# Kernel optimization log

Hardware: AMD Instinct MI355X
Metric: run time of the kernel (lower is better)

## Reference

```python
import jax, jax.numpy as jnp
import numpy as np

SHAPES = ((496, 432), (248, 216), (124, 108))
NS = (40000, 20000, 8000)
T = 32
B = 4
EPS = 1e-3


def _bn(x, g, b, m, v):
    return (x - m) * (g / jnp.sqrt(v + EPS)) + b


def _vfe_scale(voxels, num_pts, w1, p1, w2, p2):
    # voxels: (N, T, 4); num_pts: (N,)
    Tp = voxels.shape[1]
    n = num_pts.astype(voxels.dtype)[:, None, None]
    m3 = voxels[:, :, :3].sum(axis=1, keepdims=True) / n
    m2 = voxels[:, :, :2].sum(axis=1, keepdims=True) / n
    feat = jnp.concatenate([voxels[:, :, :4], voxels[:, :, :3] - m3, voxels[:, :, :2] - m2], axis=-1)  # (N,T,9)
    mask = (jnp.arange(Tp)[None, :] < num_pts[:, None]).astype(voxels.dtype)[:, :, None]
    x = feat
    for w, (g, b_, rm, rv) in ((w1, p1), (w2, p2)):
        h = jax.nn.relu(_bn(jnp.einsum('ntc,cd->ntd', x, w), g, b_, rm, rv))  # (N,T,64)
        gmax = h.max(axis=1, keepdims=True)  # global max includes padded rows, as in torch source
        x = jnp.concatenate([h, jnp.broadcast_to(gmax, h.shape)], axis=-1) * mask  # (N,T,128)
    return x.max(axis=1)[:, :64]  # (N,64)


def _scatter_bev(vf, coords, h, w, batch_size):
    b = coords[:, 0]
    y = jnp.clip(coords[:, 2], 0, h - 1)
    x = jnp.clip(coords[:, 3], 0, w - 1)
    grid = jnp.zeros((batch_size, vf.shape[1], h, w), vf.dtype)
    return grid.at[b, :, y, x].set(vf)


def _fusion(x, w, g, b, m, v):
    y = jax.lax.conv_general_dilated(x, w, (1, 1), ((1, 1), (1, 1)),
                                     dimension_numbers=('NCHW', 'OIHW', 'NCHW'))
    y = _bn(y, g[None, :, None, None], b[None, :, None, None], m[None, :, None, None], v[None, :, None, None])
    return jax.nn.relu(y)


def setup_inputs() -> dict:
    key = jax.random.key(0)
    ks = jax.random.split(key, 32)
    inp = {}
    for s in range(3):
        h, w = SHAPES[s]
        inp[f'voxels_{s}'] = jax.random.normal(ks[s], (NS[s], T, 4), dtype=jnp.float32)
        inp[f'num_pts_{s}'] = jax.random.randint(ks[3 + s], (NS[s],), 1, T + 1, dtype=jnp.int32)
        b = jax.random.randint(ks[6 + s], (NS[s],), 0, B, dtype=jnp.int32)
        z = jnp.zeros((NS[s],), jnp.int32)
        y = jax.random.randint(ks[9 + s], (NS[s],), 0, h, dtype=jnp.int32)
        x = jax.random.randint(ks[12 + s], (NS[s],), 0, w, dtype=jnp.int32)
        inp[f'coords_{s}'] = jnp.stack([b, z, y, x], axis=1)
    # VFE params (stacked across the 3 scales; identical shapes per scale)
    inp['w1'] = jax.random.normal(ks[15], (3, 9, 64), dtype=jnp.float32) * 0.1
    inp['g1'] = jnp.ones((3, 64), jnp.float32) + 0.1 * jax.random.normal(ks[16], (3, 64))
    inp['b1'] = 0.05 * jax.random.normal(ks[17], (3, 64))
    inp['rm1'] = 0.05 * jax.random.normal(ks[18], (3, 64))
    inp['rv1'] = 0.5 + jnp.abs(jax.random.normal(ks[19], (3, 64)))
    inp['w2'] = jax.random.normal(ks[20], (3, 128, 64), dtype=jnp.float32) * 0.05
    inp['g2'] = jnp.ones((3, 64), jnp.float32) + 0.1 * jax.random.normal(ks[21], (3, 64))
    inp['b2'] = 0.05 * jax.random.normal(ks[22], (3, 64))
    inp['rm2'] = 0.05 * jax.random.normal(ks[23], (3, 64))
    inp['rv2'] = 0.5 + jnp.abs(jax.random.normal(ks[24], (3, 64)))
    # Fusion convs (2): Conv2d(128,64,3) + BN
    inp['fw'] = jax.random.normal(ks[25], (2, 64, 128, 3, 3), dtype=jnp.float32) * 0.03
    inp['fg'] = jnp.ones((2, 64), jnp.float32) + 0.1 * jax.random.normal(ks[26], (2, 64))
    inp['fb'] = 0.05 * jax.random.normal(ks[27], (2, 64))
    inp['fm'] = 0.05 * jax.random.normal(ks[28], (2, 64))
    inp['fv'] = 0.5 + jnp.abs(jax.random.normal(ks[29], (2, 64)))
    inp['batch_size'] = B
    return inp


def reference(voxels_0, voxels_1, voxels_2,
              w1, g1, b1, rm1, rv1, w2, g2, b2, rm2, rv2,
              fw, fg, fb, fm, fv,
              num_pts_0, num_pts_1, num_pts_2,
              coords_0, coords_1, coords_2, batch_size):
    voxels = (voxels_0, voxels_1, voxels_2)
    num_pts = (num_pts_0, num_pts_1, num_pts_2)
    coords = (coords_0, coords_1, coords_2)
    sf = []
    for s in range(3):
        vf = _vfe_scale(voxels[s], num_pts[s],
                        w1[s], (g1[s], b1[s], rm1[s], rv1[s]),
                        w2[s], (g2[s], b2[s], rm2[s], rv2[s]))
        h, w = SHAPES[s]
        sf.append(_scatter_bev(vf, coords[s], h, w, batch_size))
    # bottom-up fusion: scale2 -> scale1 -> scale0
    up = jax.image.resize(sf[2], sf[1].shape[:2] + SHAPES[1], method='bilinear')
    fused_1 = _fusion(jnp.concatenate([sf[1], up], axis=1), fw[1], fg[1], fb[1], fm[1], fv[1])
    up = jax.image.resize(fused_1, fused_1.shape[:2] + SHAPES[0], method='bilinear')
    fused_0 = _fusion(jnp.concatenate([sf[0], up], axis=1), fw[0], fg[0], fb[0], fm[0], fv[0])
    return fused_0  # spatial_features_2d: (B, 64, 496, 432)
```

## Files before the change

kernel.cpp:

```cpp
#include <hip/hip_runtime.h>

typedef unsigned short u16;
typedef short bf16x8 __attribute__((ext_vector_type(8)));
typedef float f32x4 __attribute__((ext_vector_type(4)));

#define EPSV 1e-3f

__device__ __forceinline__ float bf2f(u16 u) {
  union { unsigned int i; float f; } x; x.i = ((unsigned int)u) << 16; return x.f;
}
__device__ __forceinline__ u16 f2bf(float f) {
  union { float f; unsigned int i; } x; x.f = f;
  unsigned int r = x.i + 0x7fffu + ((x.i >> 16) & 1u);
  return (u16)(r >> 16);
}

#define WAVE_FENCE() do { __builtin_amdgcn_s_waitcnt(0); __builtin_amdgcn_wave_barrier(); } while (0)

__global__ void twt_kernel(const float* __restrict__ fw, u16* __restrict__ fwT) {
  int i = blockIdx.x * blockDim.x + threadIdx.x;
  if (i >= 2 * 4 * 9 * 64 * 32) return;
  int ciq = i & 31;
  int r = i >> 5;
  int co = r & 63; r >>= 6;
  int tap = r % 9; r /= 9;
  int qk = r & 3;
  int set = r >> 2;
  int ci = qk * 32 + ciq;
  fwT[i] = f2bf(fw[(((set * 64 + co) * 128 + ci) * 9) + tap]);
}

__global__ __launch_bounds__(256, 2) void vfe_mfma_kernel(
    const float* __restrict__ vox, const int* __restrict__ npts,
    const float* __restrict__ w1, const float* __restrict__ g1, const float* __restrict__ b1,
    const float* __restrict__ rm1, const float* __restrict__ rv1,
    const float* __restrict__ w2, const float* __restrict__ g2, const float* __restrict__ b2,
    const float* __restrict__ rm2, const float* __restrict__ rv2,
    float* __restrict__ vf, int N)
{
  struct PerWave {
    u16 X[32 * 72];
    u16 F[32 * 40];
    u16 G[64];
  };
  __shared__ __align__(16) union {
    struct { u16 W1T[64 * 40]; u16 W2T[64 * 136]; } w;
    PerWave r[4];
  } lds;

  const int tid = threadIdx.x;
  const int lane = tid & 63;
  const int wv = tid >> 6;
  const int m16 = lane & 15;
  const int q = lane >> 4;

  for (int i = tid; i < 64 * 40; i += 256) {
    int c = i / 40, k = i % 40;
    lds.w.W1T[i] = f2bf(k < 9 ? w1[k * 64 + c] : 0.f);
  }
  for (int i = tid; i < 64 * 136; i += 256) {
    int c = i / 136, j = i % 136;
    lds.w.W2T[i] = f2bf(j < 128 ? w2[j * 64 + c] : 0.f);
  }
  __syncthreads();

  bf16x8 bW1[4], bLo[4][2], bHi[4][2];
  float sc1[4], sh1[4], sc2[4], sh2[4];
#pragma unroll
  for (int nf = 0; nf < 4; ++nf) {
    int c = nf * 16 + m16;
    bW1[nf] = *(const bf16x8*)&lds.w.W1T[c * 40 + q * 8];
#pragma unroll
    for (int ks = 0; ks < 2; ++ks) {
      bLo[nf][ks] = *(const bf16x8*)&lds.w.W2T[c * 136 + ks * 32 + q * 8];
      bHi[nf][ks] = *(const bf16x8*)&lds.w.W2T[c * 136 + 64 + ks * 32 + q * 8];
    }
    float s1 = g1[c] * rsqrtf(rv1[c] + EPSV);
    sc1[nf] = s1; sh1[nf] = b1[c] - rm1[c] * s1;
    float s2 = g2[c] * rsqrtf(rv2[c] + EPSV);
    sc2[nf] = s2; sh2[nf] = b2[c] - rm2[c] * s2;
  }
  __syncthreads();

  u16* X = lds.r[wv].X;
  u16* F = lds.r[wv].F;
  u16* G = lds.r[wv].G;
  for (int i = lane; i < 640; i += 64) ((unsigned int*)F)[i] = 0u;

  const int wgid = blockIdx.x * 4 + wv;
  const int wstride = gridDim.x * 4;

  for (int v = wgid; v < N; v += wstride) {
    const int n = npts[v];
    float px = 0.f, py = 0.f, pz = 0.f, pw = 0.f;
    if (lane < 32) {
      float4 u = *(const float4*)(vox + ((size_t)v * 32 + lane) * 4);
      px = u.x; py = u.y; pz = u.z; pw = u.w;
    }
    float sx = px, sy = py, sz = pz;
#pragma unroll
    for (int off = 32; off >= 1; off >>= 1) {
      sx += __shfl_xor(sx, off);
      sy += __shfl_xor(sy, off);
      sz += __shfl_xor(sz, off);
    }
    float nf_ = (float)n;
    float mx = sx / nf_, my = sy / nf_, mz = sz / nf_;
    if (lane < 32) {
      float dx = px - mx, dy = py - my, dz = pz - mz;
      bf16x8 r0, r1;
      r0[0] = (short)f2bf(px); r0[1] = (short)f2bf(py);
      r0[2] = (short)f2bf(pz); r0[3] = (short)f2bf(pw);
      r0[4] = (short)f2bf(dx); r0[5] = (short)f2bf(dy);
      r0[6] = (short)f2bf(dz); r0[7] = (short)f2bf(dx);
      r1 = (bf16x8){0, 0, 0, 0, 0, 0, 0, 0};
      r1[0] = (short)f2bf(dy);
      *(bf16x8*)&F[lane * 40 + 0] = r0;
      *(bf16x8*)&F[lane * 40 + 8] = r1;
    }
    WAVE_FENCE();

    bf16x8 a1[2];
    a1[0] = *(const bf16x8*)&F[m16 * 40 + q * 8];
    a1[1] = *(const bf16x8*)&F[(16 + m16) * 40 + q * 8];
    f32x4 acc1[2][4];
#pragma unroll
    for (int mf = 0; mf < 2; ++mf)
#pragma unroll
      for (int nf = 0; nf < 4; ++nf) {
        acc1[mf][nf] = (f32x4){0.f, 0.f, 0.f, 0.f};
        acc1[mf][nf] = __builtin_amdgcn_mfma_f32_16x16x32_bf16(a1[mf], bW1[nf], acc1[mf][nf], 0, 0, 0);
      }

    float gmx[4] = {0.f, 0.f, 0.f, 0.f};
#pragma unroll
    for (int mf = 0; mf < 2; ++mf)
#pragma unroll
      for (int nf = 0; nf < 4; ++nf)
#pragma unroll
        for (int r = 0; r < 4; ++r) {
          float h = fmaxf(acc1[mf][nf][r] * sc1[nf] + sh1[nf], 0.f);
          gmx[nf] = fmaxf(gmx[nf], h);
          int t = mf * 16 + q * 4 + r;
          X[t * 72 + nf * 16 + m16] = f2bf(h);
        }
#pragma unroll
    for (int nf = 0; nf < 4; ++nf) {
      gmx[nf] = fmaxf(gmx[nf], __shfl_xor(gmx[nf], 16));
      gmx[nf] = fmaxf(gmx[nf], __shfl_xor(gmx[nf], 32));
    }
    if (q == 0) {
#pragma unroll
      for (int nf = 0; nf < 4; ++nf) G[nf * 16 + m16] = f2bf(gmx[nf]);
    }
    WAVE_FENCE();

    f32x4 ga[4];
#pragma unroll
    for (int nf = 0; nf < 4; ++nf) ga[nf] = (f32x4){0.f, 0.f, 0.f, 0.f};
#pragma unroll
    for (int ks = 0; ks < 2; ++ks) {
      bf16x8 ag = (bf16x8){0, 0, 0, 0, 0, 0, 0, 0};
      if (m16 == 0) ag = *(const bf16x8*)&G[ks * 32 + q * 8];
#pragma unroll
      for (int nf = 0; nf < 4; ++nf)
        ga[nf] = __builtin_amdgcn_mfma_f32_16x16x32_bf16(ag, bHi[nf][ks], ga[nf], 0, 0, 0);
    }
    float gt[4];
#pragma unroll
    for (int nf = 0; nf < 4; ++nf) {
      float s = ga[nf][0] + ga[nf][1] + ga[nf][2] + ga[nf][3];
      s += __shfl_xor(s, 16);
      s += __shfl_xor(s, 32);
      gt[nf] = s;
    }

    f32x4 acc2[2][4];
#pragma unroll
    for (int mf = 0; mf < 2; ++mf)
#pragma unroll
      for (int nf = 0; nf < 4; ++nf)
        acc2[mf][nf] = (f32x4){gt[nf], gt[nf], gt[nf], gt[nf]};
#pragma unroll
    for (int ks = 0; ks < 2; ++ks) {
      bf16x8 a2[2];
      a2[0] = *(const bf16x8*)&X[m16 * 72 + ks * 32 + q * 8];
      a2[1] = *(const bf16x8*)&X[(16 + m16) * 72 + ks * 32 + q * 8];
#pragma unroll
      for (int mf = 0; mf < 2; ++mf)
#pragma unroll
        for (int nf = 0; nf < 4; ++nf)
          acc2[mf][nf] = __builtin_amdgcn_mfma_f32_16x16x32_bf16(a2[mf], bLo[nf][ks], acc2[mf][nf], 0, 0, 0);
    }

    float vm[4] = {0.f, 0.f, 0.f, 0.f};
#pragma unroll
    for (int mf = 0; mf < 2; ++mf)
#pragma unroll
      for (int nf = 0; nf < 4; ++nf)
#pragma unroll
        for (int r = 0; r < 4; ++r) {
          int t = mf * 16 + q * 4 + r;
          float h2 = fmaxf(acc2[mf][nf][r] * sc2[nf] + sh2[nf], 0.f);
          if (t < n) vm[nf] = fmaxf(vm[nf], h2);
        }
#pragma unroll
    for (int nf = 0; nf < 4; ++nf) {
      vm[nf] = fmaxf(vm[nf], __shfl_xor(vm[nf], 16));
      vm[nf] = fmaxf(vm[nf], __shfl_xor(vm[nf], 32));
    }
    float outv = (q == 0) ? vm[0] : (q == 1) ? vm[1] : (q == 2) ? vm[2] : vm[3];
    vf[(size_t)v * 64 + q * 16 + m16] = outv;
    __builtin_amdgcn_wave_barrier();
  }
}

__global__ void winner_kernel(const int* __restrict__ coords, int* __restrict__ win,
                              int N, int H, int W) {
  int v = blockIdx.x * blockDim.x + threadIdx.x;
  if (v >= N) return;
  int b = coords[v * 4 + 0];
  int y = min(max(coords[v * 4 + 2], 0), H - 1);
  int x = min(max(coords[v * 4 + 3], 0), W - 1);
  atomicMax(&win[(b * H + y) * W + x], v);
}

__global__ void fill_kernel(const int* __restrict__ win, const float* __restrict__ vf,
                            u16* __restrict__ dst, int cells, size_t ps, int planar) {
  int i = blockIdx.x * blockDim.x + threadIdx.x;
  if (i >= cells * 8) return;
  int cell = i >> 3, c8 = (i & 7) * 8;
  int wv = win[cell];
  bf16x8 o = (bf16x8){0, 0, 0, 0, 0, 0, 0, 0};
  if (wv >= 0) {
    const float* p = vf + (size_t)wv * 64 + c8;
    float4 v0 = *(const float4*)p;
    float4 v1 = *(const float4*)(p + 4);
    o[0] = (short)f2bf(v0.x); o[1] = (short)f2bf(v0.y);
    o[2] = (short)f2bf(v0.z); o[3] = (short)f2bf(v0.w);
    o[4] = (short)f2bf(v1.x); o[5] = (short)f2bf(v1.y);
    o[6] = (short)f2bf(v1.z); o[7] = (short)f2bf(v1.w);
  }
  u16* d = planar ? (dst + (size_t)(c8 >> 5) * ps + (size_t)cell * 32 + (c8 & 31))
                  : (dst + (size_t)cell * 64 + c8);
  *(bf16x8*)d = o;
}

__global__ void upsample_kernel(const u16* __restrict__ src, u16* __restrict__ dst,
                                int Hc, int Wc, size_t ps, int total8) {
  int i = blockIdx.x * blockDim.x + threadIdx.x;
  if (i >= total8) return;
  int c8 = (i & 7) * 8;
  int px = i >> 3;
  int W2 = Wc * 2, H2 = Hc * 2;
  int x = px % W2; int t = px / W2; int y = t % H2; int n = t / H2;
  int ky = y >> 1, kx = x >> 1;
  int ya, yb, xa, xb; float wya, wxa;
  if ((y & 1) == 0) { ya = ky > 0 ? ky - 1 : 0; yb = ky; wya = 0.25f; }
  else              { ya = ky; yb = (ky + 1 < Hc) ? ky + 1 : Hc - 1; wya = 0.75f; }
  if ((x & 1) == 0) { xa = kx > 0 ? kx - 1 : 0; xb = kx; wxa = 0.25f; }
  else              { xa = kx; xb = (kx + 1 < Wc) ? kx + 1 : Wc - 1; wxa = 0.75f; }
  float wyb = 1.f - wya, wxb = 1.f - wxa;
  const u16* sp = src + c8;
  bf16x8 vaa = *(const bf16x8*)&sp[((size_t)(n * Hc + ya) * Wc + xa) * 64];
  bf16x8 vab = *(const bf16x8*)&sp[((size_t)(n * Hc + ya) * Wc + xb) * 64];
  bf16x8 vba = *(const bf16x8*)&sp[((size_t)(n * Hc + yb) * Wc + xa) * 64];
  bf16x8 vbb = *(const bf16x8*)&sp[((size_t)(n * Hc + yb) * Wc + xb) * 64];
  bf16x8 o;
#pragma unroll
  for (int j = 0; j < 8; ++j) {
    float v = wya * (wxa * bf2f((u16)vaa[j]) + wxb * bf2f((u16)vab[j])) +
              wyb * (wxa * bf2f((u16)vba[j]) + wxb * bf2f((u16)vbb[j]));
    o[j] = (short)f2bf(v);
  }
  *(bf16x8*)&dst[(size_t)(2 + (c8 >> 5)) * ps + (size_t)px * 32 + (c8 & 31)] = o;
}

template<int H, int W, bool NCHW_OUT>
__global__ __launch_bounds__(256, 3) void conv_kernel(
    const u16* __restrict__ in, const u16* __restrict__ wT,
    const float* __restrict__ fg, const float* __restrict__ fb,
    const float* __restrict__ fm, const float* __restrict__ fv,
    void* __restrict__ outv)
{
  constexpr int XT = 32, YT = 8;
  constexpr int XTILES = (W + XT - 1) / XT;
  constexpr int YTILES = H / YT;
  constexpr int HC = XT + 2;
  constexpr int NPX = (YT + 2) * HC;
  const size_t PS = (size_t)4 * H * W * 32;
  __shared__ __align__(16) union {
    struct { char A[(NPX / 2) * 128]; char B[2][4096]; } s;
    float T[4 * 32 * 33];
  } lds;

  const int tid = threadIdx.x;
  const int lane = tid & 63;
  const int wv = tid >> 6;
  const int m16 = lane & 15;
  const int q = lane >> 4;

  int bid = blockIdx.x;
  const int xt = bid % XTILES; bid /= XTILES;
  const int yt = bid % YTILES;
  const int n = bid / YTILES;
  const int x0 = xt * XT, y0 = yt * YT;

  int lin[4];
#pragma unroll
  for (int mf = 0; mf < 4; ++mf)
    lin[mf] = (2 * wv + (mf >> 1)) * HC + ((mf & 1) << 4) + m16;

  const int bbase = ((m16 >> 1) << 7) + (((((m16 & 1) << 2) + q) ^ ((m16 >> 1) & 7)) << 4);

  f32x4 acc[4][4];
#pragma unroll
  for (int mf = 0; mf < 4; ++mf)
#pragma unroll
    for (int nf = 0; nf < 4; ++nf)
      acc[mf][nf] = (f32x4){0.f, 0.f, 0.f, 0.f};

  const int bco = tid >> 2, bs = tid & 3;
  const int bslot = ((((bco & 1) << 2) + bs) ^ ((bco >> 1) & 7));
  const int bldst = ((bco >> 1) << 7) + (bslot << 4);
  const int bgsrc = bco * 32 + bs * 8;

  for (int qk = 0; qk < 4; ++qk) {
    const u16* inq = in + (size_t)qk * PS;
    const u16* wq = wT + qk * (9 * 64 * 32);
    {
#pragma unroll
      for (int it = 0; it < 6; ++it) {
        int c = tid + it * 256;
        if (c < NPX * 4) {
          int p = c >> 2, s = c & 3;
          int r = p / HC, xx = p - r * HC;
          int gy = y0 - 1 + r, gx = x0 - 1 + xx;
          uint4 v = make_uint4(0, 0, 0, 0);
          if (gy >= 0 && gy < H && gx >= 0 && gx < W)
            v = *(const uint4*)(inq + ((size_t)((n * H + gy) * W + gx)) * 32 + s * 8);
          int slot = (((p & 1) << 2) + s) ^ ((p >> 1) & 7);
          *(uint4*)(lds.s.A + ((p >> 1) << 7) + (slot << 4)) = v;
        }
      }
      uint4 v = *(const uint4*)(wq + bgsrc);
      *(uint4*)(lds.s.B[0] + bldst) = v;
    }
    __syncthreads();

#pragma unroll
    for (int tap = 0; tap < 9; ++tap) {
      uint4 bv;
      if (tap < 8) bv = *(const uint4*)(wq + (tap + 1) * 2048 + bgsrc);
      const int tapofs = (tap / 3) * HC + (tap % 3);
      const char* Bb = lds.s.B[tap & 1];
      bf16x8 b[4], a[4];
#pragma unroll
      for (int nf = 0; nf < 4; ++nf)
        b[nf] = *(const bf16x8*)(Bb + (nf << 10) + bbase);
#pragma unroll
      for (int mf = 0; mf < 4; ++mf) {
        int hp = lin[mf] + tapofs;
        int slot = (((hp & 1) << 2) + q) ^ ((hp >> 1) & 7);
        a[mf] = *(const bf16x8*)(lds.s.A + ((hp >> 1) << 7) + (slot << 4));
      }
#pragma unroll
      for (int mf = 0; mf < 4; ++mf)
#pragma unroll
        for (int nf = 0; nf < 4; ++nf)
          acc[mf][nf] = __builtin_amdgcn_mfma_f32_16x16x32_bf16(a[mf], b[nf], acc[mf][nf], 0, 0, 0);
      if (tap < 8) *(uint4*)(lds.s.B[(tap + 1) & 1] + bldst) = bv;
      __syncthreads();
    }
  }

  float sc[4], sh[4];
#pragma unroll
  for (int nf = 0; nf < 4; ++nf) {
    int co = nf * 16 + m16;
    float s = fg[co] * rsqrtf(fv[co] + EPSV);
    sc[nf] = s;
    sh[nf] = fb[co] - fm[co] * s;
  }

  if (!NCHW_OUT) {
    u16* out = (u16*)outv;
#pragma unroll
    for (int mf = 0; mf < 4; ++mf) {
      int y = y0 + wv * 2 + (mf >> 1);
#pragma unroll
      for (int nf = 0; nf < 4; ++nf)
#pragma unroll
        for (int r = 0; r < 4; ++r) {
          int px = ((mf & 1) << 4) + q * 4 + r;
          int x = x0 + px;
          if (x < W) {
            int co = nf * 16 + m16;
            float v = fmaxf(acc[mf][nf][r] * sc[nf] + sh[nf], 0.f);
            out[((size_t)(n * H + y) * W + x) * 64 + co] = f2bf(v);
          }
        }
    }
  } else {
    __syncthreads();
    float* out = (float*)outv;
    float* T = &lds.T[wv * 32 * 33];
#pragma unroll
    for (int rr = 0; rr < 2; ++rr) {
      int y = y0 + wv * 2 + rr;
#pragma unroll
      for (int half = 0; half < 2; ++half) {
#pragma unroll
        for (int nfh = 0; nfh < 2; ++nfh) {
          int nf = half * 2 + nfh;
#pragma unroll
          for (int xc = 0; xc < 2; ++xc) {
            int mf = rr * 2 + xc;
#pragma unroll
            for (int r = 0; r < 4; ++r) {
              int px = (xc << 4) + q * 4 + r;
              int col = nfh * 16 + m16;
              T[col * 33 + px] = fmaxf(acc[mf][nf][r] * sc[nf] + sh[nf], 0.f);
            }
          }
        }
        WAVE_FENCE();
        const int px = lane & 31, co2 = lane >> 5;
        int x = x0 + px;
#pragma unroll 4
        for (int it = 0; it < 16; ++it) {
          int col = it * 2 + co2;
          int co = half * 32 + col;
          float v = T[col * 33 + px];
          if (x < W) out[((size_t)(n * 64 + co) * H + y) * W + x] = v;
        }
        WAVE_FENCE();
      }
    }
  }
}

extern "C" void kernel_launch(void* const* d_in, const int* in_sizes, int n_in,
                              void* d_out, int out_size, void* d_ws, size_t ws_size,
                              hipStream_t stream) {
  int I_vox[3], I_np[3], I_co[3];
  int I_w1, I_g1, I_b1, I_rm1, I_rv1, I_w2, I_g2, I_b2, I_rm2, I_rv2;
  int I_fw, I_fg, I_fb, I_fm, I_fv;
  if (in_sizes[1] == 40000) {
    I_vox[0] = 0; I_np[0] = 1; I_co[0] = 2;
    I_vox[1] = 3; I_np[1] = 4; I_co[1] = 5;
    I_vox[2] = 6; I_np[2] = 7; I_co[2] = 8;
    I_w1 = 9; I_g1 = 10; I_b1 = 11; I_rm1 = 12; I_rv1 = 13;
    I_w2 = 14; I_g2 = 15; I_b2 = 16; I_rm2 = 17; I_rv2 = 18;
    I_fw = 19; I_fg = 20; I_fb = 21; I_fm = 22; I_fv = 23;
  } else {
    I_vox[0] = 0; I_vox[1] = 1; I_vox[2] = 2;
    I_w1 = 3; I_g1 = 4; I_b1 = 5; I_rm1 = 6; I_rv1 = 7;
    I_w2 = 8; I_g2 = 9; I_b2 = 10; I_rm2 = 11; I_rv2 = 12;
    I_fw = 13; I_fg = 14; I_fb = 15; I_fm = 16; I_fv = 17;
    I_np[0] = 18; I_np[1] = 19; I_np[2] = 20;
    I_co[0] = 21; I_co[1] = 22; I_co[2] = 23;
  }

  const int HS[3] = {496, 248, 124};
  const int WS[3] = {432, 216, 108};
  int Nv[3];
  for (int s = 0; s < 3; ++s) Nv[s] = in_sizes[I_np[s]];

  char* wsp = (char*)d_ws;
  size_t off = 0;
  auto take = [&](size_t bytes) -> void* {
    void* p = wsp + off;
    off = (off + bytes + 255) & ~(size_t)255;
    return p;
  };
  float* vf[3]; int* win[3];
  for (int s = 0; s < 3; ++s) vf[s] = (float*)take((size_t)Nv[s] * 64 * 4);
  int cells[3];
  for (int s = 0; s < 3; ++s) {
    cells[s] = 4 * HS[s] * WS[s];
    win[s] = (int*)take((size_t)cells[s] * 4);
  }
  u16* buf0 = (u16*)take((size_t)cells[0] * 128 * 2);
  u16* buf1 = (u16*)take((size_t)cells[1] * 128 * 2);
  u16* g2b  = (u16*)take((size_t)cells[2] * 64 * 2);
  u16* fus1 = (u16*)take((size_t)cells[1] * 64 * 2);
  u16* fwT  = (u16*)take((size_t)2 * 4 * 9 * 64 * 32 * 2);

  const float* W1 = (const float*)d_in[I_w1];
  const float* G1 = (const float*)d_in[I_g1];
  const float* B1 = (const float*)d_in[I_b1];
  const float* RM1 = (const float*)d_in[I_rm1];
  const float* RV1 = (const float*)d_in[I_rv1];
  const float* W2 = (const float*)d_in[I_w2];
  const float* G2 = (const float*)d_in[I_g2];
  const float* B2 = (const float*)d_in[I_b2];
  const float* RM2 = (const float*)d_in[I_rm2];
  const float* RV2 = (const float*)d_in[I_rv2];
  const float* FW = (const float*)d_in[I_fw];
  const float* FG = (const float*)d_in[I_fg];
  const float* FB = (const float*)d_in[I_fb];
  const float* FM = (const float*)d_in[I_fm];
  const float* FV = (const float*)d_in[I_fv];

  for (int s = 0; s < 3; ++s)
    hipMemsetAsync(win[s], 0xFF, (size_t)cells[s] * 4, stream);

  twt_kernel<<<(2 * 4 * 9 * 64 * 32 + 255) / 256, 256, 0, stream>>>(FW, fwT);

  for (int s = 0; s < 3; ++s) {
    int blocks = (Nv[s] + 3) / 4;
    if (blocks > 1024) blocks = 1024;
    vfe_mfma_kernel<<<blocks, 256, 0, stream>>>(
        (const float*)d_in[I_vox[s]], (const int*)d_in[I_np[s]],
        W1 + s * 9 * 64, G1 + s * 64, B1 + s * 64, RM1 + s * 64, RV1 + s * 64,
        W2 + s * 128 * 64, G2 + s * 64, B2 + s * 64, RM2 + s * 64, RV2 + s * 64,
        vf[s], Nv[s]);
  }
  for (int s = 0; s < 3; ++s) {
    winner_kernel<<<(Nv[s] + 255) / 256, 256, 0, stream>>>(
        (const int*)d_in[I_co[s]], win[s], Nv[s], HS[s], WS[s]);
  }
  const size_t ps0 = (size_t)cells[0] * 32;
  const size_t ps1 = (size_t)cells[1] * 32;
  fill_kernel<<<(cells[0] * 8 + 255) / 256, 256, 0, stream>>>(win[0], vf[0], buf0, cells[0], ps0, 1);
  fill_kernel<<<(cells[1] * 8 + 255) / 256, 256, 0, stream>>>(win[1], vf[1], buf1, cells[1], ps1, 1);
  fill_kernel<<<(cells[2] * 8 + 255) / 256, 256, 0, stream>>>(win[2], vf[2], g2b, cells[2], 0, 0);

  {
    int total8 = cells[1] * 8;
    upsample_kernel<<<(total8 + 255) / 256, 256, 0, stream>>>(g2b, buf1, 124, 108, ps1, total8);
  }
  conv_kernel<248, 216, false><<<4 * (248 / 8) * 7, 256, 0, stream>>>(
      buf1, fwT + 4 * 9 * 64 * 32, FG + 64, FB + 64, FM + 64, FV + 64, fus1);
  {
    int total8 = cells[0] * 8;
    upsample_kernel<<<(total8 + 255) / 256, 256, 0, stream>>>(fus1, buf0, 248, 216, ps0, total8);
  }
  conv_kernel<496, 432, true><<<4 * (496 / 8) * 14, 256, 0, stream>>>(
      buf0, fwT, FG, FB, FM, FV, (float*)d_out);
}
```

Baseline: 765.0 us.

## Merge weight transpose, VFE scales and winner scatter into one launch

Folds the weight-transpose kernel, the three per-scale VFE kernels and the three winner atomicMax kernels into a single kernel, routing blocks to each role by block index. The three fill kernels become one, and the three memsets become one over a single concatenated winner buffer. The aim is to cut launch count and per-launch tail and idle time, and to let independent stages run concurrently. In exchange the fused kernel uses VFE-sized shared memory for every block, 2-block occupancy bounds for all roles, and a fixed wave stride of 4096. The winner blocks are independent of the VFE output, so running them concurrently is safe.

```diff
diff --git a/kernel.cpp b/kernel.cpp
--- a/kernel.cpp
+++ b/kernel.cpp
@@ -17,20 +17,17 @@
 
 #define WAVE_FENCE() do { __builtin_amdgcn_s_waitcnt(0); __builtin_amdgcn_wave_barrier(); } while (0)
 
-__global__ void twt_kernel(const float* __restrict__ fw, u16* __restrict__ fwT) {
-  int i = blockIdx.x * blockDim.x + threadIdx.x;
-  if (i >= 2 * 4 * 9 * 64 * 32) return;
-  int ciq = i & 31;
-  int r = i >> 5;
-  int co = r & 63; r >>= 6;
-  int tap = r % 9; r /= 9;
-  int qk = r & 3;
-  int set = r >> 2;
-  int ci = qk * 32 + ciq;
-  fwT[i] = f2bf(fw[(((set * 64 + co) * 128 + ci) * 9) + tap]);
-}
-
-__global__ __launch_bounds__(256, 2) void vfe_mfma_kernel(
+struct VfePerWave {
+  u16 X[32 * 72];
+  u16 F[32 * 40];
+  u16 G[64];
+};
+union VfeLds {
+  struct { u16 W1T[64 * 40]; u16 W2T[64 * 136]; } w;
+  VfePerWave r[4];
+};
+
+__device__ void vfe_body(VfeLds& lds, int lb,
     const float* __restrict__ vox, const int* __restrict__ npts,
     const float* __restrict__ w1, const float* __restrict__ g1, const float* __restrict__ b1,
     const float* __restrict__ rm1, const float* __restrict__ rv1,
@@ -38,16 +35,6 @@
     const float* __restrict__ rm2, const float* __restrict__ rv2,
     float* __restrict__ vf, int N)
 {
-  struct PerWave {
-    u16 X[32 * 72];
-    u16 F[32 * 40];
-    u16 G[64];
-  };
-  __shared__ __align__(16) union {
-    struct { u16 W1T[64 * 40]; u16 W2T[64 * 136]; } w;
-    PerWave r[4];
-  } lds;
-
   const int tid = threadIdx.x;
   const int lane = tid & 63;
   const int wv = tid >> 6;
@@ -87,8 +74,8 @@
   u16* G = lds.r[wv].G;
   for (int i = lane; i < 640; i += 64) ((unsigned int*)F)[i] = 0u;
 
-  const int wgid = blockIdx.x * 4 + wv;
-  const int wstride = gridDim.x * 4;
+  const int wgid = lb * 4 + wv;
+  const int wstride = 4096;
 
   for (int v = wgid; v < N; v += wstride) {
     const int n = npts[v];
@@ -215,22 +202,81 @@
   }
 }
 
-__global__ void winner_kernel(const int* __restrict__ coords, int* __restrict__ win,
-                              int N, int H, int W) {
-  int v = blockIdx.x * blockDim.x + threadIdx.x;
-  if (v >= N) return;
-  int b = coords[v * 4 + 0];
+__global__ __launch_bounds__(256, 2) void fused1_kernel(
+    const float* __restrict__ fw, u16* __restrict__ fwT,
+    const float* __restrict__ vox0, const float* __restrict__ vox1, const float* __restrict__ vox2,
+    const int* __restrict__ np0, const int* __restrict__ np1, const int* __restrict__ np2,
+    const float* __restrict__ W1, const float* __restrict__ G1, const float* __restrict__ B1,
+    const float* __restrict__ RM1, const float* __restrict__ RV1,
+    const float* __restrict__ W2, const float* __restrict__ G2, const float* __restrict__ B2,
+    const float* __restrict__ RM2, const float* __restrict__ RV2,
+    float* __restrict__ vf0, float* __restrict__ vf1, float* __restrict__ vf2,
+    const int* __restrict__ co0, const int* __restrict__ co1, const int* __restrict__ co2,
+    int* __restrict__ win,
+    int N0, int N1, int N2)
+{
+  __shared__ __align__(16) VfeLds vlds;
+  int b = blockIdx.x;
+  const int tid = threadIdx.x;
+
+  if (b < 576) {
+    int i = b * 256 + tid;
+    int ciq = i & 31;
+    int r = i >> 5;
+    int co = r & 63; r >>= 6;
+    int tap = r % 9; r /= 9;
+    int qk = r & 3;
+    int set = r >> 2;
+    int ci = qk * 32 + ciq;
+    fwT[i] = f2bf(fw[(((set * 64 + co) * 128 + ci) * 9) + tap]);
+    return;
+  }
+  b -= 576;
+  if (b < 3072) {
+    int s = b >> 10, lb = b & 1023;
+    const float* vox = (s == 0) ? vox0 : (s == 1) ? vox1 : vox2;
+    const int* npts = (s == 0) ? np0 : (s == 1) ? np1 : np2;
+    float* vf = (s == 0) ? vf0 : (s == 1) ? vf1 : vf2;
+    int N = (s == 0) ? N0 : (s == 1) ? N1 : N2;
+    vfe_body(vlds, lb, vox, npts,
+             W1 + s * 576, G1 + s * 64, B1 + s * 64, RM1 + s * 64, RV1 + s * 64,
+             W2 + s * 8192, G2 + s * 64, B2 + s * 64, RM2 + s * 64, RV2 + s * 64,
+             vf, N);
+    return;
+  }
+  b -= 3072;
+  int t = b * 256 + tid;
+  if (t >= N0 + N1 + N2) return;
+  const int* coords; int H, W; int* wn; int v;
+  if (t < N0)            { coords = co0; H = 496; W = 432; wn = win; v = t; }
+  else if (t < N0 + N1)  { coords = co1; H = 248; W = 216; wn = win + 4 * 496 * 432; v = t - N0; }
+  else                   { coords = co2; H = 124; W = 108; wn = win + 4 * 496 * 432 + 4 * 248 * 216; v = t - N0 - N1; }
+  int bb = coords[v * 4 + 0];
   int y = min(max(coords[v * 4 + 2], 0), H - 1);
   int x = min(max(coords[v * 4 + 3], 0), W - 1);
-  atomicMax(&win[(b * H + y) * W + x], v);
-}
-
-__global__ void fill_kernel(const int* __restrict__ win, const float* __restrict__ vf,
-                            u16* __restrict__ dst, int cells, size_t ps, int planar) {
+  atomicMax(&wn[(bb * H + y) * W + x], v);
+}
+
+__global__ void fillf_kernel(const int* __restrict__ win,
+                             const float* __restrict__ vf0, const float* __restrict__ vf1,
+                             const float* __restrict__ vf2,
+                             u16* __restrict__ buf0, u16* __restrict__ buf1, u16* __restrict__ g2b,
+                             int c0, int c1, int c2, size_t ps0, size_t ps1) {
   int i = blockIdx.x * blockDim.x + threadIdx.x;
-  if (i >= cells * 8) return;
-  int cell = i >> 3, c8 = (i & 7) * 8;
-  int wv = win[cell];
+  if (i >= (c0 + c1 + c2) * 8) return;
+  int cellg = i >> 3, c8 = (i & 7) * 8;
+  int wv = win[cellg];
+  const float* vf; u16* d;
+  if (cellg < c0) {
+    vf = vf0;
+    d = buf0 + (size_t)(c8 >> 5) * ps0 + (size_t)cellg * 32 + (c8 & 31);
+  } else if (cellg < c0 + c1) {
+    vf = vf1;
+    d = buf1 + (size_t)(c8 >> 5) * ps1 + (size_t)(cellg - c0) * 32 + (c8 & 31);
+  } else {
+    vf = vf2;
+    d = g2b + (size_t)(cellg - c0 - c1) * 64 + c8;
+  }
   bf16x8 o = (bf16x8){0, 0, 0, 0, 0, 0, 0, 0};
   if (wv >= 0) {
     const float* p = vf + (size_t)wv * 64 + c8;
@@ -241,8 +287,6 @@
     o[4] = (short)f2bf(v1.x); o[5] = (short)f2bf(v1.y);
     o[6] = (short)f2bf(v1.z); o[7] = (short)f2bf(v1.w);
   }
-  u16* d = planar ? (dst + (size_t)(c8 >> 5) * ps + (size_t)cell * 32 + (c8 & 31))
-                  : (dst + (size_t)cell * 64 + c8);
   *(bf16x8*)d = o;
 }
 
@@ -474,13 +518,12 @@
     off = (off + bytes + 255) & ~(size_t)255;
     return p;
   };
-  float* vf[3]; int* win[3];
+  float* vf[3];
   for (int s = 0; s < 3; ++s) vf[s] = (float*)take((size_t)Nv[s] * 64 * 4);
   int cells[3];
-  for (int s = 0; s < 3; ++s) {
-    cells[s] = 4 * HS[s] * WS[s];
-    win[s] = (int*)take((size_t)cells[s] * 4);
-  }
+  for (int s = 0; s < 3; ++s) cells[s] = 4 * HS[s] * WS[s];
+  int cellsTot = cells[0] + cells[1] + cells[2];
+  int* win = (int*)take((size_t)cellsTot * 4);
   u16* buf0 = (u16*)take((size_t)cells[0] * 128 * 2);
   u16* buf1 = (u16*)take((size_t)cells[1] * 128 * 2);
   u16* g2b  = (u16*)take((size_t)cells[2] * 64 * 2);
@@ -503,29 +546,24 @@
   const float* FM = (const float*)d_in[I_fm];
   const float* FV = (const float*)d_in[I_fv];
 
-  for (int s = 0; s < 3; ++s)
-    hipMemsetAsync(win[s], 0xFF, (size_t)cells[s] * 4, stream);
-
-  twt_kernel<<<(2 * 4 * 9 * 64 * 32 + 255) / 256, 256, 0, stream>>>(FW, fwT);
-
-  for (int s = 0; s < 3; ++s) {
-    int blocks = (Nv[s] + 3) / 4;
-    if (blocks > 1024) blocks = 1024;
-    vfe_mfma_kernel<<<blocks, 256, 0, stream>>>(
-        (const float*)d_in[I_vox[s]], (const int*)d_in[I_np[s]],
-        W1 + s * 9 * 64, G1 + s * 64, B1 + s * 64, RM1 + s * 64, RV1 + s * 64,
-        W2 + s * 128 * 64, G2 + s * 64, B2 + s * 64, RM2 + s * 64, RV2 + s * 64,
-        vf[s], Nv[s]);
-  }
-  for (int s = 0; s < 3; ++s) {
-    winner_kernel<<<(Nv[s] + 255) / 256, 256, 0, stream>>>(
-        (const int*)d_in[I_co[s]], win[s], Nv[s], HS[s], WS[s]);
-  }
+  hipMemsetAsync(win, 0xFF, (size_t)cellsTot * 4, stream);
+
+  {
+    int winB = (Nv[0] + Nv[1] + Nv[2] + 255) / 256;
+    fused1_kernel<<<576 + 3072 + winB, 256, 0, stream>>>(
+        FW, fwT,
+        (const float*)d_in[I_vox[0]], (const float*)d_in[I_vox[1]], (const float*)d_in[I_vox[2]],
+        (const int*)d_in[I_np[0]], (const int*)d_in[I_np[1]], (const int*)d_in[I_np[2]],
+        W1, G1, B1, RM1, RV1, W2, G2, B2, RM2, RV2,
+        vf[0], vf[1], vf[2],
+        (const int*)d_in[I_co[0]], (const int*)d_in[I_co[1]], (const int*)d_in[I_co[2]],
+        win, Nv[0], Nv[1], Nv[2]);
+  }
+
   const size_t ps0 = (size_t)cells[0] * 32;
   const size_t ps1 = (size_t)cells[1] * 32;
-  fill_kernel<<<(cells[0] * 8 + 255) / 256, 256, 0, stream>>>(win[0], vf[0], buf0, cells[0], ps0, 1);
-  fill_kernel<<<(cells[1] * 8 + 255) / 256, 256, 0, stream>>>(win[1], vf[1], buf1, cells[1], ps1, 1);
-  fill_kernel<<<(cells[2] * 8 + 255) / 256, 256, 0, stream>>>(win[2], vf[2], g2b, cells[2], 0, 0);
+  fillf_kernel<<<(cellsTot * 8 + 255) / 256, 256, 0, stream>>>(
+      win, vf[0], vf[1], vf[2], buf0, buf1, g2b, cells[0], cells[1], cells[2], ps0, ps1);
 
   {
     int total8 = cells[1] * 8;
```

Result: faster. 711.2 us (-7.0%).
